# Optimization experiments

Measured on AMD Instinct MI355X. Metric: run time of the kernel, lower is better.

Reference implementation:

```python
import jax, jax.numpy as jnp
import numpy as np

ALPHA = 0.8  # LeakyReLU negative slope
OUT_DIM = 128
EDGE_DIM = 64


def setup_inputs() -> dict:
    key = jax.random.key(0)
    ks = jax.random.split(key, 6)
    N, NS, IN, OUT, ED = 25000, 32, 128, OUT_DIM, EDGE_DIM
    return {
        "input": jax.random.normal(ks[0], (N, IN), jnp.float32),
        "neigh_feat": jax.random.normal(ks[1], (N * NS, IN), jnp.float32),
        "edge_emb": jax.random.normal(ks[2], (N * NS, ED), jnp.float32),
        "mask": jnp.zeros((N,), jnp.int32),  # unused by forward, kept for signature fidelity
        "W": jax.random.normal(ks[3], (IN, OUT), jnp.float32) * 0.1,
        "W2": jax.random.normal(ks[4], (IN, OUT), jnp.float32) * 0.1,
        "a": jax.random.normal(ks[5], (2 * OUT + ED, 1), jnp.float32) * 0.1,
    }


def reference(input, neigh_feat, edge_emb, mask, W, W2, a):
    N = input.shape[0]
    ns = neigh_feat.shape[0] // N
    out_dim = W.shape[1]
    ed = edge_emb.shape[1]

    x = input @ W                                   # [N, out]
    neighs = (neigh_feat @ W2).reshape(N, ns, out_dim)  # [N, ns, out]
    edge = edge_emb.reshape(N, ns, ed)              # [N, ns, ed]

    # a_input @ a decomposed: avoid materializing the repeated/concatenated tensor.
    a_x = a[:out_dim, 0]
    a_n = a[out_dim:2 * out_dim, 0]
    a_e = a[2 * out_dim:, 0]
    scores = (x @ a_x)[:, None] + neighs @ a_n + edge @ a_e  # [N, ns]
    e = jnp.where(scores > 0, scores, ALPHA * scores)        # LeakyReLU(alpha)

    attention = jax.nn.softmax(e, axis=1)           # softmax over neighbors
    # dropout p=0.0 (eval) -> identity

    h_prime = jnp.einsum("ns,nsd->nd", attention, neighs)  # [N, out]
    output = jnp.concatenate([x, h_prime], axis=1)          # concat_node
    e_agg = jnp.einsum("ns,nse->ne", attention, edge)       # concat_edge
    output = jnp.concatenate([output, e_agg], axis=1)       # [N, 2*out+ed]
    return jax.nn.elu(output)
```

## Files before the change

kernel.cpp:

```cpp
#include <hip/hip_runtime.h>
#include <hip/hip_bf16.h>
#include <math.h>

typedef __bf16 bf16_t;
typedef __attribute__((ext_vector_type(8))) __bf16 bf16x8;
typedef __attribute__((ext_vector_type(4))) float f32x4;
typedef __attribute__((ext_vector_type(2))) float f32x2;

#define NB 8

__global__ __launch_bounds__(256) void pack_weights_kernel(
    const float* __restrict__ W, const float* __restrict__ W2,
    const float* __restrict__ a,
    bf16_t* __restrict__ Wp, bf16_t* __restrict__ W2p,
    float* __restrict__ w2an) {
  int idx = blockIdx.x * 256 + threadIdx.x;
  int j  = idx & 7;
  int l  = (idx >> 3) & 63;
  int nt = (idx >> 9) & 7;
  int kt = idx >> 12;
  int k   = kt * 32 + (l >> 4) * 8 + j;
  int col = nt * 16 + (l & 15);
  Wp[idx]  = (bf16_t)W[k * 128 + col];
  W2p[idx] = (bf16_t)W2[k * 128 + col];
  if (blockIdx.x == 0 && threadIdx.x < 128) {
    const float* r = W2 + threadIdx.x * 128;
    float s = 0.f;
    for (int c = 0; c < 128; ++c) s += r[c] * a[128 + c];
    w2an[threadIdx.x] = s;
  }
}

__global__ __launch_bounds__(256) void gemm_kernel(
    const float* __restrict__ src, const bf16_t* __restrict__ Wpk,
    const float* __restrict__ a,
    float* __restrict__ out, float* __restrict__ sxv, int col_off, int N) {
  __shared__ __align__(16) bf16_t As[32 * 128];
  __shared__ float sp2[2][32];
  const int t  = threadIdx.x;
  const int rb = blockIdx.x * 32;
  const int w = t >> 6, l = t & 63;

  for (int c = t; c < 512; c += 256) {
    int row = c >> 4;
    int kc  = (c & 15) * 8;
    int grow = rb + row;
    float v[8];
    if (grow < N) {
      const f32x4* p = (const f32x4*)(src + (size_t)grow * 128 + kc);
      f32x4 v0 = p[0], v1 = p[1];
      v[0]=v0[0]; v[1]=v0[1]; v[2]=v0[2]; v[3]=v0[3];
      v[4]=v1[0]; v[5]=v1[1]; v[6]=v1[2]; v[7]=v1[3];
    } else {
      for (int j = 0; j < 8; ++j) v[j] = 0.f;
    }
    bf16x8 b;
    for (int j = 0; j < 8; ++j) b[j] = (bf16_t)v[j];
    *(bf16x8*)(&As[row * 128 + (kc ^ ((row & 7) << 3))]) = b;
  }
  __syncthreads();

  const int mt = w & 1;
  const int ntg = (w >> 1) * 4;
  const int arow = mt * 16 + (l & 15);

  f32x4 acc[4] = {};
#pragma unroll
  for (int kt = 0; kt < 4; ++kt) {
    bf16x8 af = *(const bf16x8*)(&As[arow * 128 + ((kt * 32 + (l >> 4) * 8) ^ ((arow & 7) << 3))]);
#pragma unroll
    for (int i = 0; i < 4; ++i) {
      bf16x8 bfv = *(const bf16x8*)(&Wpk[((kt * 8 + (ntg + i)) * 64 + l) * 8]);
      acc[i] = __builtin_amdgcn_mfma_f32_16x16x32_bf16(af, bfv, acc[i], 0, 0, 0);
    }
  }

  if (sxv) {
    float ax[4];
#pragma unroll
    for (int i = 0; i < 4; ++i) ax[i] = a[(ntg + i) * 16 + (l & 15)];
#pragma unroll
    for (int j = 0; j < 4; ++j) {
      float p = acc[0][j]*ax[0] + acc[1][j]*ax[1] + acc[2][j]*ax[2] + acc[3][j]*ax[3];
      p += __shfl_xor(p, 1); p += __shfl_xor(p, 2);
      p += __shfl_xor(p, 4); p += __shfl_xor(p, 8);
      if ((l & 15) == 0) sp2[w >> 1][mt * 16 + (l >> 4) * 4 + j] = p;
    }
    __syncthreads();
    if (t < 32) {
      int gr = rb + t;
      if (gr < N) sxv[gr] = sp2[0][t] + sp2[1][t];
    }
  }

#pragma unroll
  for (int i = 0; i < 4; ++i) {
    int col = (ntg + i) * 16 + (l & 15);
#pragma unroll
    for (int j = 0; j < 4; ++j) {
      int row = mt * 16 + (l >> 4) * 4 + j;
      int gr = rb + row;
      if (gr < N) {
        float v = acc[i][j];
        v = v > 0.f ? v : __expf(v) - 1.f;
        __builtin_nontemporal_store(v, &out[(size_t)gr * 320 + col_off + col]);
      }
    }
  }
}

__global__ __launch_bounds__(256) void node_kernel(
    const float* __restrict__ neigh_feat, const float* __restrict__ edge_emb,
    const float* __restrict__ a, const float* __restrict__ w2an,
    const float* __restrict__ sxv, float* __restrict__ aggbuf,
    float* __restrict__ out) {
  const int t = threadIdx.x;
  const int w = t >> 6, l = t & 63;
  const int n0 = blockIdx.x * NB;
  const int r = t >> 3, sub = t & 7;
  const int c0 = sub * 16;

  __shared__ __align__(16) bf16_t As[2][32 * 128];
  __shared__ __align__(16) bf16_t Eb[2][32 * 64];
  __shared__ float srow[2][32];

  const f32x4 wn0 = *(const f32x4*)(w2an + c0);
  const f32x4 wn1 = *(const f32x4*)(w2an + c0 + 4);
  const f32x4 wn2 = *(const f32x4*)(w2an + c0 + 8);
  const f32x4 wn3 = *(const f32x4*)(w2an + c0 + 12);
  const f32x4 ae0 = *(const f32x4*)(a + 256 + sub * 8);
  const f32x4 ae1 = *(const f32x4*)(a + 256 + sub * 8 + 4);

  const int wrA = r * 128 + (((sub * 2) ^ (r & 7)) * 8);
  const int wrB = r * 128 + ((((sub * 2) + 1) ^ (r & 7)) * 8);
  const int wrE = r * 64 + ((sub ^ (r & 7)) * 8);

  f32x4 nA0, nA1, nA2, nA3, eA0, eA1;
  f32x4 nB0, nB1, nB2, nB3, eB0, eB1;

#define ISSUE(P, node_) do {                                               \
    const float* nf_ = neigh_feat + (size_t)(node_) * 4096 + r * 128 + c0; \
    n##P##0 = *(const f32x4*)(nf_);                                        \
    n##P##1 = *(const f32x4*)(nf_ + 4);                                    \
    n##P##2 = *(const f32x4*)(nf_ + 8);                                    \
    n##P##3 = *(const f32x4*)(nf_ + 12);                                   \
    const float* ee_ = edge_emb + (size_t)(node_) * 2048 + r * 64 + sub * 8; \
    e##P##0 = *(const f32x4*)(ee_);                                        \
    e##P##1 = *(const f32x4*)(ee_ + 4);                                    \
  } while (0)

#define BODY(P, b, kk) do {                                                 \
    const int node = n0 + (kk);                                             \
    {                                                                       \
      float p = n##P##0[0]*wn0[0] + n##P##0[1]*wn0[1] + n##P##0[2]*wn0[2] + n##P##0[3]*wn0[3] \
              + n##P##1[0]*wn1[0] + n##P##1[1]*wn1[1] + n##P##1[2]*wn1[2] + n##P##1[3]*wn1[3] \
              + n##P##2[0]*wn2[0] + n##P##2[1]*wn2[1] + n##P##2[2]*wn2[2] + n##P##2[3]*wn2[3] \
              + n##P##3[0]*wn3[0] + n##P##3[1]*wn3[1] + n##P##3[2]*wn3[2] + n##P##3[3]*wn3[3] \
              + e##P##0[0]*ae0[0] + e##P##0[1]*ae0[1] + e##P##0[2]*ae0[2] + e##P##0[3]*ae0[3] \
              + e##P##1[0]*ae1[0] + e##P##1[1]*ae1[1] + e##P##1[2]*ae1[2] + e##P##1[3]*ae1[3]; \
      p += __shfl_xor(p, 1); p += __shfl_xor(p, 2); p += __shfl_xor(p, 4);  \
      if (sub == 0) srow[b][r] = p;                                         \
      bf16x8 x0, x1, xe;                                                    \
      _Pragma("unroll")                                                     \
      for (int j = 0; j < 4; ++j) {                                         \
        x0[j] = (bf16_t)n##P##0[j]; x0[j+4] = (bf16_t)n##P##1[j];           \
        x1[j] = (bf16_t)n##P##2[j]; x1[j+4] = (bf16_t)n##P##3[j];           \
        xe[j] = (bf16_t)e##P##0[j]; xe[j+4] = (bf16_t)e##P##1[j];           \
      }                                                                     \
      *(bf16x8*)(&As[b][wrA]) = x0;                                         \
      *(bf16x8*)(&As[b][wrB]) = x1;                                         \
      *(bf16x8*)(&Eb[b][wrE]) = xe;                                         \
    }                                                                       \
    if ((kk) + 2 < NB) ISSUE(P, node + 2);                                  \
    __syncthreads();                                                        \
    float av;                                                               \
    {                                                                       \
      const float sx = sxv[node];                                           \
      float e = srow[b][l & 31] + sx;                                       \
      e = e > 0.f ? e : 0.8f * e;                                           \
      float m = e;                                                          \
      m = fmaxf(m, __shfl_xor(m, 1));                                       \
      m = fmaxf(m, __shfl_xor(m, 2));                                       \
      m = fmaxf(m, __shfl_xor(m, 4));                                       \
      m = fmaxf(m, __shfl_xor(m, 8));                                       \
      m = fmaxf(m, __shfl_xor(m, 16));                                      \
      float pe = __expf(e - m);                                             \
      float s2 = pe;                                                        \
      s2 += __shfl_xor(s2, 1);                                              \
      s2 += __shfl_xor(s2, 2);                                              \
      s2 += __shfl_xor(s2, 4);                                              \
      s2 += __shfl_xor(s2, 8);                                              \
      s2 += __shfl_xor(s2, 16);                                             \
      av = pe / s2;                                                         \
    }                                                                       \
    if (w == 0) {                                                           \
      const int gg = l >> 2, boff = (l & 3) * 4;                            \
      const char* base = (const char*)As[b];                                \
      float a0 = 0.f, a1 = 0.f;                                             \
      _Pragma("unroll")                                                     \
      for (int s = 0; s < 32; ++s) {                                        \
        unsigned u = *(const unsigned*)(base + s * 256 + ((gg ^ (s & 7)) * 16) + boff); \
        float as = __shfl(av, s);                                           \
        a0 = fmaf(as, __uint_as_float(u << 16), a0);                        \
        a1 = fmaf(as, __uint_as_float(u & 0xffff0000u), a1);                \
      }                                                                     \
      f32x2 st = {a0, a1};                                                  \
      *(f32x2*)(aggbuf + (size_t)node * 128 + 2 * l) = st;                  \
    } else if (w == 1 && l < 32) {                                          \
      const int gg = l >> 2, boff = (l & 3) * 4;                            \
      const char* base = (const char*)Eb[b];                                \
      float a0 = 0.f, a1 = 0.f;                                             \
      _Pragma("unroll")                                                     \
      for (int s = 0; s < 32; ++s) {                                        \
        unsigned u = *(const unsigned*)(base + s * 128 + ((gg ^ (s & 7)) * 16) + boff); \
        float as = __shfl(av, s);                                           \
        a0 = fmaf(as, __uint_as_float(u << 16), a0);                        \
        a1 = fmaf(as, __uint_as_float(u & 0xffff0000u), a1);                \
      }                                                                     \
      a0 = a0 > 0.f ? a0 : __expf(a0) - 1.f;                                \
      a1 = a1 > 0.f ? a1 : __expf(a1) - 1.f;                                \
      f32x2 st = {a0, a1};                                                  \
      __builtin_nontemporal_store(st, (f32x2*)(out + (size_t)node * 320 + 256 + 2 * l)); \
    }                                                                       \
  } while (0)

  ISSUE(A, n0);
  ISSUE(B, n0 + 1);

#pragma unroll 1
  for (int k = 0; k < NB; k += 2) {
    BODY(A, 0, k);
    BODY(B, 1, k + 1);
  }
#undef BODY
#undef ISSUE
}

extern "C" void kernel_launch(void* const* d_in, const int* in_sizes, int n_in,
                              void* d_out, int out_size, void* d_ws, size_t ws_size,
                              hipStream_t stream) {
  const float* input = (const float*)d_in[0];
  const float* neigh = (const float*)d_in[1];
  const float* edge  = (const float*)d_in[2];
  const float* W     = (const float*)d_in[4];
  const float* W2    = (const float*)d_in[5];
  const float* a     = (const float*)d_in[6];
  float* out = (float*)d_out;

  const int N = in_sizes[0] / 128;

  bf16_t* W2p  = (bf16_t*)d_ws;
  bf16_t* Wp   = W2p + 16384;
  float*  w2an = (float*)((char*)d_ws + 65536);
  float*  sxv  = (float*)((char*)d_ws + 66560);
  float*  agg  = (float*)((char*)d_ws + 262144);

  pack_weights_kernel<<<64, 256, 0, stream>>>(W, W2, a, Wp, W2p, w2an);
  gemm_kernel<<<(N + 31) / 32, 256, 0, stream>>>(input, Wp, a, out, sxv, 0, N);
  node_kernel<<<N / NB, 256, 0, stream>>>(neigh, edge, a, w2an, sxv, agg, out);
  gemm_kernel<<<(N + 31) / 32, 256, 0, stream>>>(agg, W2p, a, out, nullptr, 128, N);
}
```

Before: 164.9 us.

## Distribute attention-weighted aggregation across all waves in registers instead of LDS bf16

Rewrites the per-node aggregation so each thread holds contiguous float4 slices of the neighbor and edge rows and computes its partial weighted sums in fp32 registers. Cross-wave partials are reduced through a small shared buffer. This replaces the old scheme, where rows were staged as bf16 in LDS and only one or two waves did the 32-step reduction. The intent is to remove the serial single-wave reduction and the bf16 conversion and staging, at the cost of more shuffles and an extra shared-memory reduction step per node.

Result: no change. 163.8 us (-0.6%).

```diff
diff --git a/kernel.cpp b/kernel.cpp
--- a/kernel.cpp
+++ b/kernel.cpp
@@ -5,7 +5,6 @@
 typedef __bf16 bf16_t;
 typedef __attribute__((ext_vector_type(8))) __bf16 bf16x8;
 typedef __attribute__((ext_vector_type(4))) float f32x4;
-typedef __attribute__((ext_vector_type(2))) float f32x2;
 
 #define NB 8
 
@@ -117,111 +116,120 @@
   const int t = threadIdx.x;
   const int w = t >> 6, l = t & 63;
   const int n0 = blockIdx.x * NB;
-  const int r = t >> 3, sub = t & 7;
-  const int c0 = sub * 16;
-
-  __shared__ __align__(16) bf16_t As[2][32 * 128];
-  __shared__ __align__(16) bf16_t Eb[2][32 * 64];
-  __shared__ float srow[2][32];
-
-  const f32x4 wn0 = *(const f32x4*)(w2an + c0);
-  const f32x4 wn1 = *(const f32x4*)(w2an + c0 + 4);
-  const f32x4 wn2 = *(const f32x4*)(w2an + c0 + 8);
-  const f32x4 wn3 = *(const f32x4*)(w2an + c0 + 12);
-  const f32x4 ae0 = *(const f32x4*)(a + 256 + sub * 8);
-  const f32x4 ae1 = *(const f32x4*)(a + 256 + sub * 8 + 4);
-
-  const int wrA = r * 128 + (((sub * 2) ^ (r & 7)) * 8);
-  const int wrB = r * 128 + ((((sub * 2) + 1) ^ (r & 7)) * 8);
-  const int wrE = r * 64 + ((sub ^ (r & 7)) * 8);
-
-  f32x4 nA0, nA1, nA2, nA3, eA0, eA1;
-  f32x4 nB0, nB1, nB2, nB3, eB0, eB1;
-
-#define ISSUE(P, node_) do {                                               \
-    const float* nf_ = neigh_feat + (size_t)(node_) * 4096 + r * 128 + c0; \
-    n##P##0 = *(const f32x4*)(nf_);                                        \
-    n##P##1 = *(const f32x4*)(nf_ + 4);                                    \
-    n##P##2 = *(const f32x4*)(nf_ + 8);                                    \
-    n##P##3 = *(const f32x4*)(nf_ + 12);                                   \
-    const float* ee_ = edge_emb + (size_t)(node_) * 2048 + r * 64 + sub * 8; \
-    e##P##0 = *(const f32x4*)(ee_);                                        \
-    e##P##1 = *(const f32x4*)(ee_ + 4);                                    \
+
+  __shared__ float srow[32];
+  __shared__ float se[32];
+  __shared__ __align__(16) f32x4 nag[4][32];
+  __shared__ __align__(16) f32x4 eag[4][16];
+
+  const int q = l & 31;
+  const int h = l >> 5;
+  const int p = l & 15;
+  const int g = l >> 4;
+
+  const f32x4 wn = *(const f32x4*)(w2an + 4 * q);
+  const f32x4 ae = *(const f32x4*)(a + 256 + 4 * p);
+
+  f32x4 nA[4], eA[2], nB[4], eB[2];
+  float sxA, sxB;
+
+#define ISSUE(P, node_) do {                                              \
+    const float* nf_ = neigh_feat + (size_t)(node_) * 4096 + 4 * t;       \
+    n##P[0] = *(const f32x4*)(nf_);                                       \
+    n##P[1] = *(const f32x4*)(nf_ + 1024);                                \
+    n##P[2] = *(const f32x4*)(nf_ + 2048);                                \
+    n##P[3] = *(const f32x4*)(nf_ + 3072);                                \
+    const float* ee_ = edge_emb + (size_t)(node_) * 2048 + 4 * t;         \
+    e##P[0] = *(const f32x4*)(ee_);                                       \
+    e##P[1] = *(const f32x4*)(ee_ + 1024);                                \
+    sx##P = sxv[node_];                                                   \
   } while (0)
 
-#define BODY(P, b, kk) do {                                                 \
-    const int node = n0 + (kk);                                             \
-    {                                                                       \
-      float p = n##P##0[0]*wn0[0] + n##P##0[1]*wn0[1] + n##P##0[2]*wn0[2] + n##P##0[3]*wn0[3] \
-              + n##P##1[0]*wn1[0] + n##P##1[1]*wn1[1] + n##P##1[2]*wn1[2] + n##P##1[3]*wn1[3] \
-              + n##P##2[0]*wn2[0] + n##P##2[1]*wn2[1] + n##P##2[2]*wn2[2] + n##P##2[3]*wn2[3] \
-              + n##P##3[0]*wn3[0] + n##P##3[1]*wn3[1] + n##P##3[2]*wn3[2] + n##P##3[3]*wn3[3] \
-              + e##P##0[0]*ae0[0] + e##P##0[1]*ae0[1] + e##P##0[2]*ae0[2] + e##P##0[3]*ae0[3] \
-              + e##P##1[0]*ae1[0] + e##P##1[1]*ae1[1] + e##P##1[2]*ae1[2] + e##P##1[3]*ae1[3]; \
-      p += __shfl_xor(p, 1); p += __shfl_xor(p, 2); p += __shfl_xor(p, 4);  \
-      if (sub == 0) srow[b][r] = p;                                         \
-      bf16x8 x0, x1, xe;                                                    \
-      _Pragma("unroll")                                                     \
-      for (int j = 0; j < 4; ++j) {                                         \
-        x0[j] = (bf16_t)n##P##0[j]; x0[j+4] = (bf16_t)n##P##1[j];           \
-        x1[j] = (bf16_t)n##P##2[j]; x1[j+4] = (bf16_t)n##P##3[j];           \
-        xe[j] = (bf16_t)e##P##0[j]; xe[j+4] = (bf16_t)e##P##1[j];           \
-      }                                                                     \
-      *(bf16x8*)(&As[b][wrA]) = x0;                                         \
-      *(bf16x8*)(&As[b][wrB]) = x1;                                         \
-      *(bf16x8*)(&Eb[b][wrE]) = xe;                                         \
-    }                                                                       \
-    if ((kk) + 2 < NB) ISSUE(P, node + 2);                                  \
-    __syncthreads();                                                        \
-    float av;                                                               \
-    {                                                                       \
-      const float sx = sxv[node];                                           \
-      float e = srow[b][l & 31] + sx;                                       \
-      e = e > 0.f ? e : 0.8f * e;                                           \
-      float m = e;                                                          \
-      m = fmaxf(m, __shfl_xor(m, 1));                                       \
-      m = fmaxf(m, __shfl_xor(m, 2));                                       \
-      m = fmaxf(m, __shfl_xor(m, 4));                                       \
-      m = fmaxf(m, __shfl_xor(m, 8));                                       \
-      m = fmaxf(m, __shfl_xor(m, 16));                                      \
-      float pe = __expf(e - m);                                             \
-      float s2 = pe;                                                        \
-      s2 += __shfl_xor(s2, 1);                                              \
-      s2 += __shfl_xor(s2, 2);                                              \
-      s2 += __shfl_xor(s2, 4);                                              \
-      s2 += __shfl_xor(s2, 8);                                              \
-      s2 += __shfl_xor(s2, 16);                                             \
-      av = pe / s2;                                                         \
-    }                                                                       \
-    if (w == 0) {                                                           \
-      const int gg = l >> 2, boff = (l & 3) * 4;                            \
-      const char* base = (const char*)As[b];                                \
-      float a0 = 0.f, a1 = 0.f;                                             \
-      _Pragma("unroll")                                                     \
-      for (int s = 0; s < 32; ++s) {                                        \
-        unsigned u = *(const unsigned*)(base + s * 256 + ((gg ^ (s & 7)) * 16) + boff); \
-        float as = __shfl(av, s);                                           \
-        a0 = fmaf(as, __uint_as_float(u << 16), a0);                        \
-        a1 = fmaf(as, __uint_as_float(u & 0xffff0000u), a1);                \
-      }                                                                     \
-      f32x2 st = {a0, a1};                                                  \
-      *(f32x2*)(aggbuf + (size_t)node * 128 + 2 * l) = st;                  \
-    } else if (w == 1 && l < 32) {                                          \
-      const int gg = l >> 2, boff = (l & 3) * 4;                            \
-      const char* base = (const char*)Eb[b];                                \
-      float a0 = 0.f, a1 = 0.f;                                             \
-      _Pragma("unroll")                                                     \
-      for (int s = 0; s < 32; ++s) {                                        \
-        unsigned u = *(const unsigned*)(base + s * 128 + ((gg ^ (s & 7)) * 16) + boff); \
-        float as = __shfl(av, s);                                           \
-        a0 = fmaf(as, __uint_as_float(u << 16), a0);                        \
-        a1 = fmaf(as, __uint_as_float(u & 0xffff0000u), a1);                \
-      }                                                                     \
-      a0 = a0 > 0.f ? a0 : __expf(a0) - 1.f;                                \
-      a1 = a1 > 0.f ? a1 : __expf(a1) - 1.f;                                \
-      f32x2 st = {a0, a1};                                                  \
-      __builtin_nontemporal_store(st, (f32x2*)(out + (size_t)node * 320 + 256 + 2 * l)); \
-    }                                                                       \
+#define BODY(P, kk) do {                                                  \
+    const int node = n0 + (kk);                                           \
+                            \
+    _Pragma("unroll")                                                     \
+    for (int j = 0; j < 4; ++j) {                                         \
+      float s = n##P[j][0]*wn[0] + n##P[j][1]*wn[1]                       \
+              + n##P[j][2]*wn[2] + n##P[j][3]*wn[3];                      \
+      s += __shfl_xor(s, 1);  s += __shfl_xor(s, 2);                      \
+      s += __shfl_xor(s, 4);  s += __shfl_xor(s, 8);                      \
+      s += __shfl_xor(s, 16);                                             \
+      if (q == 0) srow[8*j + 2*w + h] = s;                                \
+    }                                                                     \
+    _Pragma("unroll")                                                     \
+    for (int j = 0; j < 2; ++j) {                                         \
+      float s = e##P[j][0]*ae[0] + e##P[j][1]*ae[1]                       \
+              + e##P[j][2]*ae[2] + e##P[j][3]*ae[3];                      \
+      s += __shfl_xor(s, 1);  s += __shfl_xor(s, 2);                      \
+      s += __shfl_xor(s, 4);  s += __shfl_xor(s, 8);                      \
+      if (p == 0) se[16*j + 4*w + g] = s;                                 \
+    }                                                                     \
+    __syncthreads();                                                      \
+      \
+    float av;                                                             \
+    {                                                                     \
+      float e0 = srow[q] + se[q] + sx##P;                                 \
+      e0 = e0 > 0.f ? e0 : 0.8f * e0;                                     \
+      float m = e0;                                                       \
+      m = fmaxf(m, __shfl_xor(m, 1));                                     \
+      m = fmaxf(m, __shfl_xor(m, 2));                                     \
+      m = fmaxf(m, __shfl_xor(m, 4));                                     \
+      m = fmaxf(m, __shfl_xor(m, 8));                                     \
+      m = fmaxf(m, __shfl_xor(m, 16));                                    \
+      float pe = __expf(e0 - m);                                          \
+      float s2 = pe;                                                      \
+      s2 += __shfl_xor(s2, 1);                                            \
+      s2 += __shfl_xor(s2, 2);                                            \
+      s2 += __shfl_xor(s2, 4);                                            \
+      s2 += __shfl_xor(s2, 8);                                            \
+      s2 += __shfl_xor(s2, 16);                                           \
+      av = pe / s2;                                                       \
+    }                                                                     \
+                                \
+    {                                                                     \
+      f32x4 pn = {0.f, 0.f, 0.f, 0.f};                                    \
+      _Pragma("unroll")                                                   \
+      for (int j = 0; j < 4; ++j) {                                       \
+        float as = __shfl(av, 8*j + 2*w + h);                             \
+        pn += as * n##P[j];                                               \
+      }                                                                   \
+      pn[0] += __shfl_xor(pn[0], 32);                                     \
+      pn[1] += __shfl_xor(pn[1], 32);                                     \
+      pn[2] += __shfl_xor(pn[2], 32);                                     \
+      pn[3] += __shfl_xor(pn[3], 32);                                     \
+      if (h == 0) nag[w][q] = pn;                                         \
+      f32x4 pv = {0.f, 0.f, 0.f, 0.f};                                    \
+      _Pragma("unroll")                                                   \
+      for (int j = 0; j < 2; ++j) {                                       \
+        float as = __shfl(av, 16*j + 4*w + g);                            \
+        pv += as * e##P[j];                                               \
+      }                                                                   \
+      pv[0] += __shfl_xor(pv[0], 16);                                     \
+      pv[1] += __shfl_xor(pv[1], 16);                                     \
+      pv[2] += __shfl_xor(pv[2], 16);                                     \
+      pv[3] += __shfl_xor(pv[3], 16);                                     \
+      pv[0] += __shfl_xor(pv[0], 32);                                     \
+      pv[1] += __shfl_xor(pv[1], 32);                                     \
+      pv[2] += __shfl_xor(pv[2], 32);                                     \
+      pv[3] += __shfl_xor(pv[3], 32);                                     \
+      if (l < 16) eag[w][p] = pv;                                         \
+    }                                                                     \
+       \
+    if ((kk) + 2 < NB) ISSUE(P, node + 2);                                \
+    __syncthreads();                                                      \
+                                    \
+    if (t < 128) {                                                        \
+      const float* f = (const float*)nag;                                 \
+      float v = f[t] + f[128 + t] + f[256 + t] + f[384 + t];              \
+      aggbuf[(size_t)node * 128 + t] = v;                                 \
+    } else if (t < 192) {                                                 \
+      int c = t - 128;                                                    \
+      const float* f = (const float*)eag;                                 \
+      float v = f[c] + f[64 + c] + f[128 + c] + f[192 + c];               \
+      v = v > 0.f ? v : __expf(v) - 1.f;                                  \
+      __builtin_nontemporal_store(v, out + (size_t)node * 320 + 256 + c); \
+    }                                                                     \
   } while (0)
 
   ISSUE(A, n0);
@@ -229,8 +237,8 @@
 
 #pragma unroll 1
   for (int k = 0; k < NB; k += 2) {
-    BODY(A, 0, k);
-    BODY(B, 1, k + 1);
+    BODY(A, k);
+    BODY(B, k + 1);
   }
 #undef BODY
 #undef ISSUE
```
